# Optimization experiments

Hardware: AMD Instinct MI355X
Metric: run time of the kernel (lower is better)

## Reference

```python
import jax, jax.numpy as jnp
import numpy as np

B, S, H = 8, 1024, 768
NH, DH = 12, 64
F, E = 3072, 8
EPS = 1e-12

def layer_norm(x, g, b):
    mu = jnp.mean(x, axis=-1, keepdims=True)
    var = jnp.var(x, axis=-1, keepdims=True)
    return g * (x - mu) / jnp.sqrt(var + EPS) + b

def setup_inputs():
    key = jax.random.key(0)
    ks = jax.random.split(key, 20)
    std = 0.02
    d = {
        'hidden_states': jax.random.normal(ks[0], (B, S, H), jnp.float32),
        'Wq': jax.random.normal(ks[1], (H, H)) * std, 'bq': jnp.zeros((H,)),
        'Wk': jax.random.normal(ks[2], (H, H)) * std, 'bk': jnp.zeros((H,)),
        'Wv': jax.random.normal(ks[3], (H, H)) * std, 'bv': jnp.zeros((H,)),
        'Wao': jax.random.normal(ks[4], (H, H)) * std, 'bao': jnp.zeros((H,)),
        'ln1_g': jnp.ones((H,)), 'ln1_b': jnp.zeros((H,)),
        'Wr': jax.random.normal(ks[5], (H, E)) * std, 'br': jnp.zeros((E,)),
        'Wi': jax.random.normal(ks[6], (E, H, F)) * std, 'bi': jnp.zeros((E, F)),
        'Wo': jax.random.normal(ks[7], (F, H)) * std, 'bo': jnp.zeros((H,)),
        'ln2_g': jnp.ones((H,)), 'ln2_b': jnp.zeros((H,)),
    }
    return d

def reference(hidden_states, Wq, bq, Wk, bk, Wv, bv, Wao, bao, ln1_g, ln1_b,
              Wr, br, Wi, bi, Wo, bo, ln2_g, ln2_b):
    b, s, h = hidden_states.shape
    # --- self attention ---
    q = (hidden_states @ Wq + bq).reshape(b, s, NH, DH)
    k = (hidden_states @ Wk + bk).reshape(b, s, NH, DH)
    v = (hidden_states @ Wv + bv).reshape(b, s, NH, DH)
    scores = jnp.einsum('bqhd,bkhd->bhqk', q, k) / jnp.sqrt(jnp.float32(DH))
    probs = jax.nn.softmax(scores, axis=-1)
    ctx = jnp.einsum('bhqk,bkhd->bqhd', probs, v).reshape(b, s, h)
    attention_output = layer_norm(ctx @ Wao + bao + hidden_states, ln1_g, ln1_b)
    # --- router ---
    routing_scores = jax.nn.softmax(attention_output @ Wr + br, axis=-1)  # [b,s,E]
    routing_expert = jnp.argmax(routing_scores, axis=-1)  # [b,s]
    # --- expert FFN (dispatch/combine via per-expert masking) ---
    flat_x = attention_output.reshape(-1, h)          # [T,H]
    flat_e = routing_expert.reshape(-1)               # [T]
    flat_inter = jnp.zeros((b * s, F), flat_x.dtype)
    for e in range(E):
        mask = (flat_e == e)[:, None].astype(flat_x.dtype)
        y = jax.nn.gelu(flat_x @ Wi[e] + bi[e], approximate=False)
        flat_inter = flat_inter + mask * y
    inter = flat_inter.reshape(b, s, F)
    # --- output (dense + residual layernorm) ---
    layer_output = layer_norm(inter @ Wo + bo + attention_output, ln2_g, ln2_b)
    return layer_output, routing_scores
```

## Files before the change

### kernel.cpp

```cpp
#include <hip/hip_runtime.h>
#include <math.h>
#include <stdint.h>

#define TOKS 8192
#define HDIM 768
#define FDIM 3072
#define NEXP 8
#define NHEAD 12
#define SEQ 1024
#define BATCH 8
#define PERMSZ 9216

typedef __attribute__((ext_vector_type(8))) short s16x8;
typedef __attribute__((ext_vector_type(4))) short s16x4;
typedef __attribute__((ext_vector_type(4))) float f32x4;

__device__ __forceinline__ short f2bf(float f) {
  uint32_t u = __float_as_uint(f);
  uint32_t r = (u + 0x7fffu + ((u >> 16) & 1u)) >> 16;
  return (short)(r & 0xffffu);
}
__device__ __forceinline__ float bf2f(short h) {
  return __uint_as_float(((uint32_t)(uint16_t)h) << 16);
}
__device__ __forceinline__ void gload16(const void* g, void* l) {
  __builtin_amdgcn_global_load_lds(
      (const __attribute__((address_space(1))) uint32_t*)g,
      (__attribute__((address_space(3))) uint32_t*)l, 16, 0, 0);
}
__device__ __forceinline__ void pipe_wait_barrier() {
  asm volatile("s_waitcnt vmcnt(0)" ::: "memory");
  __builtin_amdgcn_s_barrier();
}

__global__ __launch_bounds__(256) void convert_split(
    const float* __restrict__ X, short* __restrict__ Xh, short* __restrict__ Xl, int n4)
{
  const int i = blockIdx.x * 256 + threadIdx.x;
  if (i >= n4) return;
  const float4 v = ((const float4*)X)[i];
  const float a[4] = {v.x, v.y, v.z, v.w};
  s16x4 h, l;
#pragma unroll
  for (int j = 0; j < 4; ++j) {
    h[j] = f2bf(a[j]);
    l[j] = f2bf(a[j] - bf2f(h[j]));
  }
  ((s16x4*)Xh)[i] = h;
  ((s16x4*)Xl)[i] = l;
}

__global__ __launch_bounds__(256) void transpose_split(
    const float* __restrict__ W, short* __restrict__ WTh, short* __restrict__ WTl,
    int K, int N)
{
  __shared__ float t[32][33];
  const int tid = threadIdx.x;
  const int tx = tid & 31, ty = tid >> 5;
  const int n0 = blockIdx.x * 32, k0 = blockIdx.y * 32;
#pragma unroll
  for (int r = 0; r < 4; ++r)
    t[ty + r * 8][tx] = W[(size_t)(k0 + ty + r * 8) * N + n0 + tx];
  __syncthreads();
#pragma unroll
  for (int r = 0; r < 4; ++r) {
    const float v = t[tx][ty + r * 8];
    const short h = f2bf(v);
    WTh[(size_t)(n0 + ty + r * 8) * K + k0 + tx] = h;
    WTl[(size_t)(n0 + ty + r * 8) * K + k0 + tx] = f2bf(v - bf2f(h));
  }
}

__global__ __launch_bounds__(256) void gemm_split_mfma(
    const short* __restrict__ Ah, const short* __restrict__ Al,
    const short* __restrict__ BhT, const short* __restrict__ BlT,
    const float* __restrict__ bias, float* __restrict__ C,
    int N, int K)
{
  __shared__ __align__(16) short lAh[2][4096];
  __shared__ __align__(16) short lAl[2][4096];
  __shared__ __align__(16) short lBh[2][4096];
  __shared__ __align__(16) short lBl[2][4096];
  const int tid = threadIdx.x;
  const int w = tid >> 6, lane = tid & 63;
  const int wr = w >> 1, wc = w & 1;
  const int row0 = blockIdx.y * 128, col0 = blockIdx.x * 128;
  const int sr = lane & 15, kg = lane >> 4;
  const size_t a0 = (size_t)(row0 + 2 * w * 16 + sr) * K + kg * 8;
  const size_t a1 = a0 + (size_t)16 * K;
  const size_t b0 = (size_t)(col0 + 2 * w * 16 + sr) * K + kg * 8;
  const size_t b1 = b0 + (size_t)16 * K;
  const int d0 = (2 * w) * 512, d1 = (2 * w + 1) * 512;
#define STAGE_S(bu, k0) do { \
    gload16(Ah + a0 + (k0), &lAh[bu][d0]); \
    gload16(Ah + a1 + (k0), &lAh[bu][d1]); \
    gload16(Al + a0 + (k0), &lAl[bu][d0]); \
    gload16(Al + a1 + (k0), &lAl[bu][d1]); \
    gload16(BhT + b0 + (k0), &lBh[bu][d0]); \
    gload16(BhT + b1 + (k0), &lBh[bu][d1]); \
    gload16(BlT + b0 + (k0), &lBl[bu][d0]); \
    gload16(BlT + b1 + (k0), &lBl[bu][d1]); \
  } while (0)
  f32x4 acc[4][4] = {};
  const int NT = K >> 5;
  STAGE_S(0, 0);
  pipe_wait_barrier();
  int cur = 0;
  for (int t = 0; t < NT; ++t) {
    if (t + 1 < NT) STAGE_S(cur ^ 1, (t + 1) * 32);
    s16x8 ah[4], al[4], bh[4], bl[4];
#pragma unroll
    for (int i = 0; i < 4; ++i) {
      ah[i] = *(const s16x8*)&lAh[cur][(wr * 4 + i) * 512 + lane * 8];
      al[i] = *(const s16x8*)&lAl[cur][(wr * 4 + i) * 512 + lane * 8];
      bh[i] = *(const s16x8*)&lBh[cur][(wc * 4 + i) * 512 + lane * 8];
      bl[i] = *(const s16x8*)&lBl[cur][(wc * 4 + i) * 512 + lane * 8];
    }
#pragma unroll
    for (int mi = 0; mi < 4; ++mi)
#pragma unroll
      for (int ni = 0; ni < 4; ++ni) {
        acc[mi][ni] = __builtin_amdgcn_mfma_f32_16x16x32_bf16(ah[mi], bh[ni], acc[mi][ni], 0, 0, 0);
        acc[mi][ni] = __builtin_amdgcn_mfma_f32_16x16x32_bf16(ah[mi], bl[ni], acc[mi][ni], 0, 0, 0);
        acc[mi][ni] = __builtin_amdgcn_mfma_f32_16x16x32_bf16(al[mi], bh[ni], acc[mi][ni], 0, 0, 0);
      }
    pipe_wait_barrier();
    cur ^= 1;
  }
#undef STAGE_S
  const int cl = lane & 15, rg = lane >> 4;
#pragma unroll
  for (int mi = 0; mi < 4; ++mi)
#pragma unroll
    for (int r = 0; r < 4; ++r) {
      const int row = row0 + wr * 64 + mi * 16 + rg * 4 + r;
#pragma unroll
      for (int ni = 0; ni < 4; ++ni) {
        const int c = col0 + wc * 64 + ni * 16 + cl;
        C[(size_t)row * N + c] = acc[mi][ni][r] + bias[c];
      }
    }
}

__global__ __launch_bounds__(256) void qkv_split_mfma(
    const short* __restrict__ Ah, const short* __restrict__ Al,
    const short* __restrict__ BhT, const short* __restrict__ BlT,
    const float* __restrict__ bias,
    short* __restrict__ QKh, short* __restrict__ QKl,
    short* __restrict__ VTh, short* __restrict__ VTl)
{
  const int K = 768;
  __shared__ __align__(16) short lAh[2][4096];
  __shared__ __align__(16) short lAl[2][4096];
  __shared__ __align__(16) short lBh[2][4096];
  __shared__ __align__(16) short lBl[2][4096];
  const int tid = threadIdx.x;
  const int w = tid >> 6, lane = tid & 63;
  const int wr = w >> 1, wc = w & 1;
  const int row0 = blockIdx.y * 128, col0 = blockIdx.x * 128;
  const int sr = lane & 15, kg = lane >> 4;
  const size_t a0 = (size_t)(row0 + 2 * w * 16 + sr) * K + kg * 8;
  const size_t a1 = a0 + (size_t)16 * K;
  const size_t b0 = (size_t)(col0 + 2 * w * 16 + sr) * K + kg * 8;
  const size_t b1 = b0 + (size_t)16 * K;
  const int d0 = (2 * w) * 512, d1 = (2 * w + 1) * 512;
#define STAGE_Q(bu, k0) do { \
    gload16(Ah + a0 + (k0), &lAh[bu][d0]); \
    gload16(Ah + a1 + (k0), &lAh[bu][d1]); \
    gload16(Al + a0 + (k0), &lAl[bu][d0]); \
    gload16(Al + a1 + (k0), &lAl[bu][d1]); \
    gload16(BhT + b0 + (k0), &lBh[bu][d0]); \
    gload16(BhT + b1 + (k0), &lBh[bu][d1]); \
    gload16(BlT + b0 + (k0), &lBl[bu][d0]); \
    gload16(BlT + b1 + (k0), &lBl[bu][d1]); \
  } while (0)
  f32x4 acc[4][4] = {};
  STAGE_Q(0, 0);
  pipe_wait_barrier();
  int cur = 0;
  for (int t = 0; t < 24; ++t) {
    if (t < 23) STAGE_Q(cur ^ 1, (t + 1) * 32);
    s16x8 ah[4], al[4], bh[4], bl[4];
#pragma unroll
    for (int i = 0; i < 4; ++i) {
      ah[i] = *(const s16x8*)&lAh[cur][(wr * 4 + i) * 512 + lane * 8];
      al[i] = *(const s16x8*)&lAl[cur][(wr * 4 + i) * 512 + lane * 8];
      bh[i] = *(const s16x8*)&lBh[cur][(wc * 4 + i) * 512 + lane * 8];
      bl[i] = *(const s16x8*)&lBl[cur][(wc * 4 + i) * 512 + lane * 8];
    }
#pragma unroll
    for (int mi = 0; mi < 4; ++mi)
#pragma unroll
      for (int ni = 0; ni < 4; ++ni) {
        acc[mi][ni] = __builtin_amdgcn_mfma_f32_16x16x32_bf16(ah[mi], bh[ni], acc[mi][ni], 0, 0, 0);
        acc[mi][ni] = __builtin_amdgcn_mfma_f32_16x16x32_bf16(ah[mi], bl[ni], acc[mi][ni], 0, 0, 0);
        acc[mi][ni] = __builtin_amdgcn_mfma_f32_16x16x32_bf16(al[mi], bh[ni], acc[mi][ni], 0, 0, 0);
      }
    pipe_wait_barrier();
    cur ^= 1;
  }
#undef STAGE_Q
  const int cl = lane & 15, rg = lane >> 4;
#pragma unroll
  for (int mi = 0; mi < 4; ++mi)
#pragma unroll
    for (int ni = 0; ni < 4; ++ni) {
      const int c = col0 + wc * 64 + ni * 16 + cl;
      const int rowb = row0 + wr * 64 + mi * 16 + rg * 4;
      s16x4 hv, lv;
#pragma unroll
      for (int r = 0; r < 4; ++r) {
        const float v = acc[mi][ni][r] + bias[c];
        const short hh = f2bf(v);
        hv[r] = hh;
        lv[r] = f2bf(v - bf2f(hh));
      }
      if (c < 1536) {
#pragma unroll
        for (int r = 0; r < 4; ++r) {
          QKh[(size_t)(rowb + r) * 1536 + c] = hv[r];
          QKl[(size_t)(rowb + r) * 1536 + c] = lv[r];
        }
      } else {
        const int dall = c - 1536;
        const size_t vi = (((size_t)((rowb >> 10) * NHEAD + (dall >> 6))) * 64 + (dall & 63)) * 1024
                          + (rowb & 1023);
        *(s16x4*)(VTh + vi) = hv;
        *(s16x4*)(VTl + vi) = lv;
      }
    }
}

__global__ __launch_bounds__(256, 2) void attention_part(
    const short* __restrict__ QKh, const short* __restrict__ QKl,
    const short* __restrict__ VTh, const short* __restrict__ VTl,
    float* __restrict__ O0, float* __restrict__ O1,
    float2* __restrict__ ml0, float2* __restrict__ ml1)
{
  __shared__ __align__(16) short lPh[4][2560];
  __shared__ __align__(16) short lPl[4][2560];
  const int tid = threadIdx.x;
  const int w = tid >> 6, lane = tid & 63;
  const int b = blockIdx.z, h = blockIdx.y;
  const int z = blockIdx.x & 1;
  const int q0 = (blockIdx.x >> 1) * 128 + w * 32;
  const int kv0 = z * 512;
  const int sr = lane & 15, kg = lane >> 4;
  const int cl = sr, rg = kg;
  short* myPh = lPh[w];
  short* myPl = lPl[w];
  float* Op = z ? O1 : O0;
  float2* mlp = z ? ml1 : ml0;

  s16x8 qh[2][2], ql[2][2];
  {
    const size_t qbase = ((size_t)b * SEQ + q0 + sr) * 1536 + h * 64 + kg * 8;
#pragma unroll
    for (int mi = 0; mi < 2; ++mi)
#pragma unroll
      for (int ks = 0; ks < 2; ++ks) {
        const size_t o = qbase + (size_t)mi * (16 * 1536) + ks * 32;
        qh[mi][ks] = *(const s16x8*)(QKh + o);
        ql[mi][ks] = *(const s16x8*)(QKl + o);
      }
  }
  float m_run[2][4], l_run[2][4];
#pragma unroll
  for (int mi = 0; mi < 2; ++mi)
#pragma unroll
    for (int r = 0; r < 4; ++r) { m_run[mi][r] = -3.0e38f; l_run[mi][r] = 0.f; }
  f32x4 acc_o[2][4] = {};

  for (int kt = kv0; kt < kv0 + 512; kt += 64) {
    s16x8 kh[4][2], kl2[4][2];
    {
      const size_t kbase = ((size_t)b * SEQ + kt + sr) * 1536 + 768 + h * 64 + kg * 8;
#pragma unroll
      for (int ni = 0; ni < 4; ++ni)
#pragma unroll
        for (int ks = 0; ks < 2; ++ks) {
          const size_t o = kbase + (size_t)ni * (16 * 1536) + ks * 32;
          kh[ni][ks] = *(const s16x8*)(QKh + o);
          kl2[ni][ks] = *(const s16x8*)(QKl + o);
        }
    }
    f32x4 accs[2][4] = {};
#pragma unroll
    for (int ks = 0; ks < 2; ++ks)
#pragma unroll
      for (int ni = 0; ni < 4; ++ni)
#pragma unroll
        for (int mi = 0; mi < 2; ++mi) {
          accs[mi][ni] = __builtin_amdgcn_mfma_f32_16x16x32_bf16(qh[mi][ks], kh[ni][ks], accs[mi][ni], 0, 0, 0);
          accs[mi][ni] = __builtin_amdgcn_mfma_f32_16x16x32_bf16(qh[mi][ks], kl2[ni][ks], accs[mi][ni], 0, 0, 0);
          accs[mi][ni] = __builtin_amdgcn_mfma_f32_16x16x32_bf16(ql[mi][ks], kh[ni][ks], accs[mi][ni], 0, 0, 0);
        }
    s16x8 vh[4][2], vl2[4][2];
    {
      const size_t vbase = (((size_t)(b * NHEAD + h)) * 64 + sr) * 1024 + kt + kg * 8;
#pragma unroll
      for (int nd = 0; nd < 4; ++nd)
#pragma unroll
        for (int ks2 = 0; ks2 < 2; ++ks2) {
          const size_t o = vbase + (size_t)nd * (16 * 1024) + ks2 * 32;
          vh[nd][ks2] = *(const s16x8*)(VTh + o);
          vl2[nd][ks2] = *(const s16x8*)(VTl + o);
        }
    }
#pragma unroll
    for (int mi = 0; mi < 2; ++mi)
#pragma unroll
      for (int ni = 0; ni < 4; ++ni)
#pragma unroll
        for (int r = 0; r < 4; ++r)
          accs[mi][ni][r] *= 0.125f;
#pragma unroll
    for (int mi = 0; mi < 2; ++mi)
#pragma unroll
      for (int r = 0; r < 4; ++r) {
        float mx = fmaxf(fmaxf(accs[mi][0][r], accs[mi][1][r]),
                         fmaxf(accs[mi][2][r], accs[mi][3][r]));
        mx = fmaxf(mx, __shfl_xor(mx, 1));
        mx = fmaxf(mx, __shfl_xor(mx, 2));
        mx = fmaxf(mx, __shfl_xor(mx, 4));
        mx = fmaxf(mx, __shfl_xor(mx, 8));
        const float mn = fmaxf(m_run[mi][r], mx);
        const float c = __expf(m_run[mi][r] - mn);
        m_run[mi][r] = mn;
        l_run[mi][r] *= c;
#pragma unroll
        for (int nd = 0; nd < 4; ++nd) acc_o[mi][nd][r] *= c;
        float sum = 0.f;
#pragma unroll
        for (int ni = 0; ni < 4; ++ni) {
          const float p = __expf(accs[mi][ni][r] - mn);
          sum += p;
          const short hh = f2bf(p);
          const int idx = (mi * 2 + (ni >> 1)) * 640 + (rg * 4 + r) * 40 + (ni & 1) * 16 + cl;
          myPh[idx] = hh;
          myPl[idx] = f2bf(p - bf2f(hh));
        }
        sum += __shfl_xor(sum, 1);
        sum += __shfl_xor(sum, 2);
        sum += __shfl_xor(sum, 4);
        sum += __shfl_xor(sum, 8);
        l_run[mi][r] += sum;
      }
#pragma unroll
    for (int ks2 = 0; ks2 < 2; ++ks2) {
      s16x8 pf[2], pg[2];
#pragma unroll
      for (int mi = 0; mi < 2; ++mi) {
        const int ra = (mi * 2 + ks2) * 640 + sr * 40 + kg * 8;
        pf[mi] = *(const s16x8*)&myPh[ra];
        pg[mi] = *(const s16x8*)&myPl[ra];
      }
#pragma unroll
      for (int nd = 0; nd < 4; ++nd)
#pragma unroll
        for (int mi = 0; mi < 2; ++mi) {
          acc_o[mi][nd] = __builtin_amdgcn_mfma_f32_16x16x32_bf16(pf[mi], vh[nd][ks2], acc_o[mi][nd], 0, 0, 0);
          acc_o[mi][nd] = __builtin_amdgcn_mfma_f32_16x16x32_bf16(pf[mi], vl2[nd][ks2], acc_o[mi][nd], 0, 0, 0);
          acc_o[mi][nd] = __builtin_amdgcn_mfma_f32_16x16x32_bf16(pg[mi], vh[nd][ks2], acc_o[mi][nd], 0, 0, 0);
        }
    }
  }
#pragma unroll
  for (int mi = 0; mi < 2; ++mi)
#pragma unroll
    for (int nd = 0; nd < 4; ++nd)
#pragma unroll
      for (int r = 0; r < 4; ++r) {
        const int row = q0 + mi * 16 + rg * 4 + r;
        const int d = h * 64 + nd * 16 + cl;
        Op[((size_t)b * SEQ + row) * HDIM + d] = acc_o[mi][nd][r];
      }
  if (sr == 0) {
#pragma unroll
    for (int mi = 0; mi < 2; ++mi)
#pragma unroll
      for (int r = 0; r < 4; ++r) {
        const int row = q0 + mi * 16 + rg * 4 + r;
        mlp[(size_t)(b * NHEAD + h) * SEQ + row] = make_float2(m_run[mi][r], l_run[mi][r]);
      }
  }
}

__global__ __launch_bounds__(256) void attn_combine(
    float* __restrict__ O0, const float* __restrict__ O1,
    const float2* __restrict__ ml0, const float2* __restrict__ ml1)
{
  const int t = blockIdx.x;
  const int b = t >> 10, s = t & 1023;
  const int tid = threadIdx.x;
#pragma unroll
  for (int i = 0; i < 3; ++i) {
    const int idx = tid + i * 256;
    const int h = idx >> 6;
    const float2 a0 = ml0[(size_t)(b * NHEAD + h) * SEQ + s];
    const float2 a1 = ml1[(size_t)(b * NHEAD + h) * SEQ + s];
    const float mm = fmaxf(a0.x, a1.x);
    const float w0 = __expf(a0.x - mm), w1 = __expf(a1.x - mm);
    const float denom = a0.y * w0 + a1.y * w1;
    const size_t o = (size_t)t * HDIM + idx;
    O0[o] = (O0[o] * w0 + O1[o] * w1) / denom;
  }
}

__global__ __launch_bounds__(256) void convert_bf16(
    const float* __restrict__ X, short* __restrict__ Y, int n4)
{
  const int i = blockIdx.x * 256 + threadIdx.x;
  if (i >= n4) return;
  const float4 v = ((const float4*)X)[i];
  s16x4 s;
  s[0] = f2bf(v.x); s[1] = f2bf(v.y); s[2] = f2bf(v.z); s[3] = f2bf(v.w);
  ((s16x4*)Y)[i] = s;
}

__global__ __launch_bounds__(256) void transpose_to_bf16(
    const float* __restrict__ W, short* __restrict__ WT, int K, int N)
{
  const size_t off = (size_t)blockIdx.z * (size_t)K * N;
  const float* Wp = W + off;
  short* WTp = WT + off;
  __shared__ float t[32][33];
  const int tid = threadIdx.x;
  const int tx = tid & 31, ty = tid >> 5;
  const int n0 = blockIdx.x * 32, k0 = blockIdx.y * 32;
#pragma unroll
  for (int r = 0; r < 4; ++r)
    t[ty + r * 8][tx] = Wp[(size_t)(k0 + ty + r * 8) * N + n0 + tx];
  __syncthreads();
#pragma unroll
  for (int r = 0; r < 4; ++r)
    WTp[(size_t)(n0 + ty + r * 8) * K + k0 + tx] = f2bf(t[tx][ty + r * 8]);
}

__global__ __launch_bounds__(256) void expert_up_mfma(
    const short* __restrict__ Abf, const short* __restrict__ WiT,
    const float* __restrict__ bi, const int* __restrict__ perm,
    const int* __restrict__ offs, short* __restrict__ interb)
{
  const int row0 = blockIdx.x * 128;
  if (row0 >= offs[NEXP]) return;
  int e = 0;
  while (offs[e + 1] <= row0) ++e;
  __shared__ __align__(16) short lA[2][4096];
  __shared__ __align__(16) short lB[2][4096];
  __shared__ int toks[128];
  const int tid = threadIdx.x;
  const int w = tid >> 6, lane = tid & 63;
  const int wr = w >> 1, wc = w & 1;
  const int col0 = blockIdx.y * 128;
  if (tid < 128) toks[tid] = perm[row0 + tid];
  __syncthreads();
  const int sr = lane & 15, kg = lane >> 4;
  int t0 = toks[2 * w * 16 + sr];        if (t0 < 0) t0 = toks[0];
  int t1 = toks[(2 * w + 1) * 16 + sr];  if (t1 < 0) t1 = toks[0];
  const size_t a0 = (size_t)t0 * HDIM + kg * 8;
  const size_t a1 = (size_t)t1 * HDIM + kg * 8;
  const short* Bt = WiT + (size_t)e * FDIM * HDIM;
  const size_t b0 = (size_t)(col0 + 2 * w * 16 + sr) * HDIM + kg * 8;
  const size_t b1 = b0 + (size_t)16 * HDIM;
  const int d0 = (2 * w) * 512, d1 = (2 * w + 1) * 512;
#define STAGE_E(bu, k0) do { \
    gload16(Abf + a0 + (k0), &lA[bu][d0]); \
    gload16(Abf + a1 + (k0), &lA[bu][d1]); \
    gload16(Bt + b0 + (k0), &lB[bu][d0]); \
    gload16(Bt + b1 + (k0), &lB[bu][d1]); \
  } while (0)
  f32x4 acc[4][4] = {};
  STAGE_E(0, 0);
  pipe_wait_barrier();
  int cur = 0;
  for (int t = 0; t < 24; ++t) {
    if (t < 23) STAGE_E(cur ^ 1, (t + 1) * 32);
    s16x8 af[4], bg[4];
#pragma unroll
    for (int i = 0; i < 4; ++i) {
      af[i] = *(const s16x8*)&lA[cur][(wr * 4 + i) * 512 + lane * 8];
      bg[i] = *(const s16x8*)&lB[cur][(wc * 4 + i) * 512 + lane * 8];
    }
#pragma unroll
    for (int mi = 0; mi < 4; ++mi)
#pragma unroll
      for (int ni = 0; ni < 4; ++ni)
        acc[mi][ni] = __builtin_amdgcn_mfma_f32_16x16x32_bf16(af[mi], bg[ni], acc[mi][ni], 0, 0, 0);
    pipe_wait_barrier();
    cur ^= 1;
  }
#undef STAGE_E
  const int cl = lane & 15, rg = lane >> 4;
#pragma unroll
  for (int mi = 0; mi < 4; ++mi) {
#pragma unroll
    for (int r = 0; r < 4; ++r) {
      const int rl = wr * 64 + mi * 16 + rg * 4 + r;
      const int tok = toks[rl];
      if (tok < 0) continue;
#pragma unroll
      for (int ni = 0; ni < 4; ++ni) {
        const int c = col0 + wc * 64 + ni * 16 + cl;
        float v = acc[mi][ni][r] + bi[(size_t)e * FDIM + c];
        v = 0.5f * v * (1.0f + erff(v * 0.70710678118654752f));
        interb[(size_t)tok * FDIM + c] = f2bf(v);
      }
    }
  }
}

__global__ __launch_bounds__(256) void wo_mfma(
    const short* __restrict__ Ab, const short* __restrict__ BT,
    const float* __restrict__ bias, float* __restrict__ C0, float* __restrict__ C1)
{
  __shared__ __align__(16) short lA[2][4096];
  __shared__ __align__(16) short lB[2][4096];
  const int tid = threadIdx.x;
  const int w = tid >> 6, lane = tid & 63;
  const int wr = w >> 1, wc = w & 1;
  const int row0 = blockIdx.y * 128, col0 = blockIdx.x * 128;
  const int z = blockIdx.z;
  const int kbase = z * 1536;
  const int sr = lane & 15, kg = lane >> 4;
  const size_t a0 = (size_t)(row0 + 2 * w * 16 + sr) * FDIM + kbase + kg * 8;
  const size_t a1 = a0 + (size_t)16 * FDIM;
  const size_t b0 = (size_t)(col0 + 2 * w * 16 + sr) * FDIM + kbase + kg * 8;
  const size_t b1 = b0 + (size_t)16 * FDIM;
  const int d0 = (2 * w) * 512, d1 = (2 * w + 1) * 512;
#define STAGE_W(bu, k0) do { \
    gload16(Ab + a0 + (k0), &lA[bu][d0]); \
    gload16(Ab + a1 + (k0), &lA[bu][d1]); \
    gload16(BT + b0 + (k0), &lB[bu][d0]); \
    gload16(BT + b1 + (k0), &lB[bu][d1]); \
  } while (0)
  f32x4 acc[4][4] = {};
  STAGE_W(0, 0);
  pipe_wait_barrier();
  int cur = 0;
  for (int t = 0; t < 48; ++t) {
    if (t < 47) STAGE_W(cur ^ 1, (t + 1) * 32);
    s16x8 af[4], bg[4];
#pragma unroll
    for (int i = 0; i < 4; ++i) {
      af[i] = *(const s16x8*)&lA[cur][(wr * 4 + i) * 512 + lane * 8];
      bg[i] = *(const s16x8*)&lB[cur][(wc * 4 + i) * 512 + lane * 8];
    }
#pragma unroll
    for (int mi = 0; mi < 4; ++mi)
#pragma unroll
      for (int ni = 0; ni < 4; ++ni)
        acc[mi][ni] = __builtin_amdgcn_mfma_f32_16x16x32_bf16(af[mi], bg[ni], acc[mi][ni], 0, 0, 0);
    pipe_wait_barrier();
    cur ^= 1;
  }
#undef STAGE_W
  float* C = z ? C1 : C0;
  const int cl = lane & 15, rg = lane >> 4;
#pragma unroll
  for (int mi = 0; mi < 4; ++mi) {
#pragma unroll
    for (int r = 0; r < 4; ++r) {
      const int row = row0 + wr * 64 + mi * 16 + rg * 4 + r;
#pragma unroll
      for (int ni = 0; ni < 4; ++ni) {
        const int c = col0 + wc * 64 + ni * 16 + cl;
        C[(size_t)row * HDIM + c] = acc[mi][ni][r] + (z ? 0.f : bias[c]);
      }
    }
  }
}

__global__ __launch_bounds__(256) void add_ln_kernel(
    const float* __restrict__ X, const float* __restrict__ R,
    const float* __restrict__ g, const float* __restrict__ bb,
    float* __restrict__ out)
{
  const int t = blockIdx.x;
  const int tid = threadIdx.x;
  const float* x = X + (size_t)t * HDIM;
  const float* r = R + (size_t)t * HDIM;
  float v[3];
  float sum = 0.f, ssq = 0.f;
#pragma unroll
  for (int i = 0; i < 3; ++i) {
    const float val = x[tid + i * 256] + r[tid + i * 256];
    v[i] = val;
    sum += val;
    ssq += val * val;
  }
#pragma unroll
  for (int o = 32; o > 0; o >>= 1) {
    sum += __shfl_down(sum, o);
    ssq += __shfl_down(ssq, o);
  }
  __shared__ float red[10];
  const int wid = tid >> 6, lane = tid & 63;
  if (lane == 0) { red[wid] = sum; red[4 + wid] = ssq; }
  __syncthreads();
  if (tid == 0) {
    const float s = red[0] + red[1] + red[2] + red[3];
    const float q = red[4] + red[5] + red[6] + red[7];
    const float mean = s * (1.f / HDIM);
    const float var = q * (1.f / HDIM) - mean * mean;
    red[8] = mean;
    red[9] = rsqrtf(fmaxf(var, 0.f) + 1e-12f);
  }
  __syncthreads();
  const float mean = red[8], rstd = red[9];
#pragma unroll
  for (int i = 0; i < 3; ++i) {
    const int idx = tid + i * 256;
    out[(size_t)t * HDIM + idx] = g[idx] * (v[i] - mean) * rstd + bb[idx];
  }
}

__global__ __launch_bounds__(256) void add2_ln_kernel(
    const float* __restrict__ X1, const float* __restrict__ X2,
    const float* __restrict__ R, const float* __restrict__ g,
    const float* __restrict__ bb, float* __restrict__ out)
{
  const int t = blockIdx.x;
  const int tid = threadIdx.x;
  const float* x1 = X1 + (size_t)t * HDIM;
  const float* x2 = X2 + (size_t)t * HDIM;
  const float* r = R + (size_t)t * HDIM;
  float v[3];
  float sum = 0.f, ssq = 0.f;
#pragma unroll
  for (int i = 0; i < 3; ++i) {
    const float val = x1[tid + i * 256] + x2[tid + i * 256] + r[tid + i * 256];
    v[i] = val;
    sum += val;
    ssq += val * val;
  }
#pragma unroll
  for (int o = 32; o > 0; o >>= 1) {
    sum += __shfl_down(sum, o);
    ssq += __shfl_down(ssq, o);
  }
  __shared__ float red[10];
  const int wid = tid >> 6, lane = tid & 63;
  if (lane == 0) { red[wid] = sum; red[4 + wid] = ssq; }
  __syncthreads();
  if (tid == 0) {
    const float s = red[0] + red[1] + red[2] + red[3];
    const float q = red[4] + red[5] + red[6] + red[7];
    const float mean = s * (1.f / HDIM);
    const float var = q * (1.f / HDIM) - mean * mean;
    red[8] = mean;
    red[9] = rsqrtf(fmaxf(var, 0.f) + 1e-12f);
  }
  __syncthreads();
  const float mean = red[8], rstd = red[9];
#pragma unroll
  for (int i = 0; i < 3; ++i) {
    const int idx = tid + i * 256;
    out[(size_t)t * HDIM + idx] = g[idx] * (v[i] - mean) * rstd + bb[idx];
  }
}

__global__ __launch_bounds__(256) void router_kernel(
    const float* __restrict__ X, const float* __restrict__ Wr,
    const float* __restrict__ br, float* __restrict__ scores_out,
    int* __restrict__ expert, int* __restrict__ counts)
{
  const int wid = threadIdx.x >> 6, lane = threadIdx.x & 63;
  const int tok = blockIdx.x * 4 + wid;
  const float* x = X + (size_t)tok * HDIM;
  float acc[8] = {};
  for (int k0 = 0; k0 < HDIM; k0 += 64) {
    const float xv = x[k0 + lane];
    const float* wrow = Wr + (size_t)(k0 + lane) * NEXP;
    const float4 w0 = *reinterpret_cast<const float4*>(wrow);
    const float4 w1 = *reinterpret_cast<const float4*>(wrow + 4);
    acc[0] = fmaf(xv, w0.x, acc[0]);
    acc[1] = fmaf(xv, w0.y, acc[1]);
    acc[2] = fmaf(xv, w0.z, acc[2]);
    acc[3] = fmaf(xv, w0.w, acc[3]);
    acc[4] = fmaf(xv, w1.x, acc[4]);
    acc[5] = fmaf(xv, w1.y, acc[5]);
    acc[6] = fmaf(xv, w1.z, acc[6]);
    acc[7] = fmaf(xv, w1.w, acc[7]);
  }
#pragma unroll
  for (int e = 0; e < 8; ++e)
#pragma unroll
    for (int o = 32; o > 0; o >>= 1) acc[e] += __shfl_down(acc[e], o);
  if (lane == 0) {
    float mx = -3.0e38f;
#pragma unroll
    for (int e = 0; e < 8; ++e) { acc[e] += br[e]; mx = fmaxf(mx, acc[e]); }
    float sum = 0.f;
#pragma unroll
    for (int e = 0; e < 8; ++e) { acc[e] = expf(acc[e] - mx); sum += acc[e]; }
    const float inv = 1.f / sum;
    int best = 0;
    float bv = acc[0];
#pragma unroll
    for (int e = 0; e < 8; ++e) {
      const float p = acc[e] * inv;
      scores_out[(size_t)tok * NEXP + e] = p;
      if (acc[e] > bv) { bv = acc[e]; best = e; }
    }
    expert[tok] = best;
    atomicAdd(&counts[best], 1);
  }
}

__global__ void offsets_kernel(const int* __restrict__ counts, int* __restrict__ offs)
{
  if (threadIdx.x == 0 && blockIdx.x == 0) {
    int a = 0;
    for (int e = 0; e < NEXP; ++e) {
      offs[e] = a;
      a += ((counts[e] + 127) >> 7) << 7;
    }
    offs[NEXP] = a;
  }
}

__global__ __launch_bounds__(256) void scatter_kernel(
    const int* __restrict__ expert, const int* __restrict__ offs,
    int* __restrict__ cursor, int* __restrict__ perm)
{
  const int t = blockIdx.x * 256 + threadIdx.x;
  if (t >= TOKS) return;
  const int e = expert[t];
  const int pos = atomicAdd(&cursor[e], 1);
  perm[offs[e] + pos] = t;
}

extern "C" void kernel_launch(void* const* d_in, const int* in_sizes, int n_in,
                              void* d_out, int out_size, void* d_ws, size_t ws_size,
                              hipStream_t stream) {
  const float* hidden = (const float*)d_in[0];
  const float* Wq  = (const float*)d_in[1];
  const float* bq  = (const float*)d_in[2];
  const float* Wk  = (const float*)d_in[3];
  const float* bk  = (const float*)d_in[4];
  const float* Wv  = (const float*)d_in[5];
  const float* bv  = (const float*)d_in[6];
  const float* Wao = (const float*)d_in[7];
  const float* bao = (const float*)d_in[8];
  const float* ln1g = (const float*)d_in[9];
  const float* ln1b = (const float*)d_in[10];
  const float* Wr  = (const float*)d_in[11];
  const float* br  = (const float*)d_in[12];
  const float* Wi  = (const float*)d_in[13];
  const float* bi  = (const float*)d_in[14];
  const float* Wo  = (const float*)d_in[15];
  const float* bo  = (const float*)d_in[16];
  const float* ln2g = (const float*)d_in[17];
  const float* ln2b = (const float*)d_in[18];

  float* out = (float*)d_out;
  float* scores_out = out + (size_t)TOKS * HDIM;

  const size_t M1 = (size_t)TOKS * HDIM;
  const size_t HW = (size_t)HDIM * HDIM;
  float* ws = (float*)d_ws;
  short* QKhb = (short*)ws;
  short* QKlb = (short*)(ws + M1);
  short* VThb = (short*)(ws + 2 * M1);
  short* VTlb = VThb + (size_t)BATCH * NHEAD * 64 * 1024;
  float* ctxb = ws + 3 * M1;
  float* Opart1 = ws + 4 * M1;
  float* bqkv = ws + 3 * M1;
  short* Hh = (short*)(ws + 4 * M1);
  short* Hl = Hh + M1;
  short* Ch = Hh; short* Cl = Hl;
  short* wt = (short*)(ws + 5 * M1);
  short* WqkvhT = wt;
  short* WqkvlT = wt + 3 * HW;
  short* WaohT  = wt + 6 * HW;
  short* WaolT  = wt + 7 * HW;
  float2* ml0 = (float2*)(ws + 5 * M1 + 4 * HW);
  float2* ml1 = ml0 + (size_t)BATCH * NHEAD * SEQ;
  float* aoproj   = ws;
  float* attn_out = ws + M1;
  float* tmp2a    = ws;
  float* tmp2b    = ws + 3 * M1;
  short* Abf    = (short*)(ws + 2 * M1);
  short* WiT    = Abf + M1;
  short* WoT    = WiT + (size_t)NEXP * FDIM * HDIM;
  short* interb = WoT + (size_t)HDIM * FDIM;
  int* ints   = (int*)(interb + (size_t)TOKS * FDIM);
  int* perm   = ints;
  int* expert = ints + PERMSZ;
  int* counts = expert + TOKS;
  int* offs   = counts + NEXP;
  int* cursor = offs + NEXP + 1;

  hipMemsetAsync(counts, 0, (NEXP + NEXP + 1 + NEXP) * sizeof(int), stream);
  hipMemsetAsync(perm, 0xFF, PERMSZ * sizeof(int), stream);
  hipMemcpyAsync(bqkv,        bq, HDIM * sizeof(float), hipMemcpyDeviceToDevice, stream);
  hipMemcpyAsync(bqkv + 768,  bk, HDIM * sizeof(float), hipMemcpyDeviceToDevice, stream);
  hipMemcpyAsync(bqkv + 1536, bv, HDIM * sizeof(float), hipMemcpyDeviceToDevice, stream);

  const dim3 blk(256);
  convert_split<<<dim3(TOKS * HDIM / 4 / 256), blk, 0, stream>>>(hidden, Hh, Hl, TOKS * HDIM / 4);
  transpose_split<<<dim3(24, 24), blk, 0, stream>>>(Wq,  WqkvhT,          WqkvlT,          HDIM, HDIM);
  transpose_split<<<dim3(24, 24), blk, 0, stream>>>(Wk,  WqkvhT + HW,     WqkvlT + HW,     HDIM, HDIM);
  transpose_split<<<dim3(24, 24), blk, 0, stream>>>(Wv,  WqkvhT + 2 * HW, WqkvlT + 2 * HW, HDIM, HDIM);
  transpose_split<<<dim3(24, 24), blk, 0, stream>>>(Wao, WaohT,           WaolT,           HDIM, HDIM);

  qkv_split_mfma<<<dim3(2304 / 128, TOKS / 128), blk, 0, stream>>>(
      Hh, Hl, WqkvhT, WqkvlT, bqkv, QKhb, QKlb, VThb, VTlb);

  attention_part<<<dim3((SEQ / 128) * 2, NHEAD, BATCH), blk, 0, stream>>>(
      QKhb, QKlb, VThb, VTlb, ctxb, Opart1, ml0, ml1);
  attn_combine<<<dim3(TOKS), blk, 0, stream>>>(ctxb, Opart1, ml0, ml1);

  convert_split<<<dim3(TOKS * HDIM / 4 / 256), blk, 0, stream>>>(ctxb, Ch, Cl, TOKS * HDIM / 4);
  gemm_split_mfma<<<dim3(HDIM / 128, TOKS / 128), blk, 0, stream>>>(
      Ch, Cl, WaohT, WaolT, bao, aoproj, HDIM, HDIM);
  add_ln_kernel<<<dim3(TOKS), blk, 0, stream>>>(aoproj, hidden, ln1g, ln1b, attn_out);

  router_kernel<<<dim3(TOKS / 4), blk, 0, stream>>>(attn_out, Wr, br, scores_out, expert, counts);
  offsets_kernel<<<dim3(1), dim3(64), 0, stream>>>(counts, offs);
  scatter_kernel<<<dim3(TOKS / 256), blk, 0, stream>>>(expert, offs, cursor, perm);

  transpose_to_bf16<<<dim3(FDIM / 32, HDIM / 32, NEXP), blk, 0, stream>>>(Wi, WiT, HDIM, FDIM);
  transpose_to_bf16<<<dim3(HDIM / 32, FDIM / 32, 1), blk, 0, stream>>>(Wo, WoT, FDIM, HDIM);
  convert_bf16<<<dim3(TOKS * HDIM / 4 / 256), blk, 0, stream>>>(attn_out, Abf, TOKS * HDIM / 4);

  expert_up_mfma<<<dim3(PERMSZ / 128, FDIM / 128), blk, 0, stream>>>(
      Abf, WiT, bi, perm, offs, interb);
  wo_mfma<<<dim3(HDIM / 128, TOKS / 128, 2), blk, 0, stream>>>(interb, WoT, bo, tmp2a, tmp2b);
  add2_ln_kernel<<<dim3(TOKS), blk, 0, stream>>>(tmp2a, tmp2b, attn_out, ln2g, ln2b, out);
}
```

Baseline: 896.9 us.

## Fuse attention combine with bf16 split, split-K output projection, direct A loads

The attention combine kernel now writes the hi/lo bf16 split of the context directly, which removes a separate fp32 store and convert pass. The output projection GEMM becomes a split-K kernel with two K halves written to separate buffers, and the existing add2 layernorm kernel sums them. The QKV and projection GEMMs now read A fragments straight from global memory into registers instead of staging them through LDS, which halves LDS traffic but relies on cache hits for the A reads. Workspace buffers are remapped so the new split outputs do not alias live data.

After: 946.6 us. 5.5% more time.

```diff
diff --git a/kernel.cpp b/kernel.cpp
--- a/kernel.cpp
+++ b/kernel.cpp
@@ -71,14 +71,14 @@
   }
 }
 
-__global__ __launch_bounds__(256) void gemm_split_mfma(
+__global__ __launch_bounds__(256) void qkv_split_mfma(
     const short* __restrict__ Ah, const short* __restrict__ Al,
     const short* __restrict__ BhT, const short* __restrict__ BlT,
-    const float* __restrict__ bias, float* __restrict__ C,
-    int N, int K)
-{
-  __shared__ __align__(16) short lAh[2][4096];
-  __shared__ __align__(16) short lAl[2][4096];
+    const float* __restrict__ bias,
+    short* __restrict__ QKh, short* __restrict__ QKl,
+    short* __restrict__ VTh, short* __restrict__ VTl)
+{
+  const int K = 768;
   __shared__ __align__(16) short lBh[2][4096];
   __shared__ __align__(16) short lBl[2][4096];
   const int tid = threadIdx.x;
@@ -86,33 +86,33 @@
   const int wr = w >> 1, wc = w & 1;
   const int row0 = blockIdx.y * 128, col0 = blockIdx.x * 128;
   const int sr = lane & 15, kg = lane >> 4;
-  const size_t a0 = (size_t)(row0 + 2 * w * 16 + sr) * K + kg * 8;
-  const size_t a1 = a0 + (size_t)16 * K;
+  size_t aoff[4];
+#pragma unroll
+  for (int i = 0; i < 4; ++i)
+    aoff[i] = (size_t)(row0 + (wr * 4 + i) * 16 + sr) * K + kg * 8;
   const size_t b0 = (size_t)(col0 + 2 * w * 16 + sr) * K + kg * 8;
   const size_t b1 = b0 + (size_t)16 * K;
   const int d0 = (2 * w) * 512, d1 = (2 * w + 1) * 512;
-#define STAGE_S(bu, k0) do { \
-    gload16(Ah + a0 + (k0), &lAh[bu][d0]); \
-    gload16(Ah + a1 + (k0), &lAh[bu][d1]); \
-    gload16(Al + a0 + (k0), &lAl[bu][d0]); \
-    gload16(Al + a1 + (k0), &lAl[bu][d1]); \
+#define STAGE_QB(bu, k0) do { \
     gload16(BhT + b0 + (k0), &lBh[bu][d0]); \
     gload16(BhT + b1 + (k0), &lBh[bu][d1]); \
     gload16(BlT + b0 + (k0), &lBl[bu][d0]); \
     gload16(BlT + b1 + (k0), &lBl[bu][d1]); \
   } while (0)
   f32x4 acc[4][4] = {};
-  const int NT = K >> 5;
-  STAGE_S(0, 0);
+  STAGE_QB(0, 0);
   pipe_wait_barrier();
   int cur = 0;
-  for (int t = 0; t < NT; ++t) {
-    if (t + 1 < NT) STAGE_S(cur ^ 1, (t + 1) * 32);
+  for (int t = 0; t < 24; ++t) {
+    if (t < 23) STAGE_QB(cur ^ 1, (t + 1) * 32);
     s16x8 ah[4], al[4], bh[4], bl[4];
 #pragma unroll
     for (int i = 0; i < 4; ++i) {
-      ah[i] = *(const s16x8*)&lAh[cur][(wr * 4 + i) * 512 + lane * 8];
-      al[i] = *(const s16x8*)&lAl[cur][(wr * 4 + i) * 512 + lane * 8];
+      ah[i] = *(const s16x8*)(Ah + aoff[i] + t * 32);
+      al[i] = *(const s16x8*)(Al + aoff[i] + t * 32);
+    }
+#pragma unroll
+    for (int i = 0; i < 4; ++i) {
       bh[i] = *(const s16x8*)&lBh[cur][(wc * 4 + i) * 512 + lane * 8];
       bl[i] = *(const s16x8*)&lBl[cur][(wc * 4 + i) * 512 + lane * 8];
     }
@@ -127,79 +127,7 @@
     pipe_wait_barrier();
     cur ^= 1;
   }
-#undef STAGE_S
-  const int cl = lane & 15, rg = lane >> 4;
-#pragma unroll
-  for (int mi = 0; mi < 4; ++mi)
-#pragma unroll
-    for (int r = 0; r < 4; ++r) {
-      const int row = row0 + wr * 64 + mi * 16 + rg * 4 + r;
-#pragma unroll
-      for (int ni = 0; ni < 4; ++ni) {
-        const int c = col0 + wc * 64 + ni * 16 + cl;
-        C[(size_t)row * N + c] = acc[mi][ni][r] + bias[c];
-      }
-    }
-}
-
-__global__ __launch_bounds__(256) void qkv_split_mfma(
-    const short* __restrict__ Ah, const short* __restrict__ Al,
-    const short* __restrict__ BhT, const short* __restrict__ BlT,
-    const float* __restrict__ bias,
-    short* __restrict__ QKh, short* __restrict__ QKl,
-    short* __restrict__ VTh, short* __restrict__ VTl)
-{
-  const int K = 768;
-  __shared__ __align__(16) short lAh[2][4096];
-  __shared__ __align__(16) short lAl[2][4096];
-  __shared__ __align__(16) short lBh[2][4096];
-  __shared__ __align__(16) short lBl[2][4096];
-  const int tid = threadIdx.x;
-  const int w = tid >> 6, lane = tid & 63;
-  const int wr = w >> 1, wc = w & 1;
-  const int row0 = blockIdx.y * 128, col0 = blockIdx.x * 128;
-  const int sr = lane & 15, kg = lane >> 4;
-  const size_t a0 = (size_t)(row0 + 2 * w * 16 + sr) * K + kg * 8;
-  const size_t a1 = a0 + (size_t)16 * K;
-  const size_t b0 = (size_t)(col0 + 2 * w * 16 + sr) * K + kg * 8;
-  const size_t b1 = b0 + (size_t)16 * K;
-  const int d0 = (2 * w) * 512, d1 = (2 * w + 1) * 512;
-#define STAGE_Q(bu, k0) do { \
-    gload16(Ah + a0 + (k0), &lAh[bu][d0]); \
-    gload16(Ah + a1 + (k0), &lAh[bu][d1]); \
-    gload16(Al + a0 + (k0), &lAl[bu][d0]); \
-    gload16(Al + a1 + (k0), &lAl[bu][d1]); \
-    gload16(BhT + b0 + (k0), &lBh[bu][d0]); \
-    gload16(BhT + b1 + (k0), &lBh[bu][d1]); \
-    gload16(BlT + b0 + (k0), &lBl[bu][d0]); \
-    gload16(BlT + b1 + (k0), &lBl[bu][d1]); \
-  } while (0)
-  f32x4 acc[4][4] = {};
-  STAGE_Q(0, 0);
-  pipe_wait_barrier();
-  int cur = 0;
-  for (int t = 0; t < 24; ++t) {
-    if (t < 23) STAGE_Q(cur ^ 1, (t + 1) * 32);
-    s16x8 ah[4], al[4], bh[4], bl[4];
-#pragma unroll
-    for (int i = 0; i < 4; ++i) {
-      ah[i] = *(const s16x8*)&lAh[cur][(wr * 4 + i) * 512 + lane * 8];
-      al[i] = *(const s16x8*)&lAl[cur][(wr * 4 + i) * 512 + lane * 8];
-      bh[i] = *(const s16x8*)&lBh[cur][(wc * 4 + i) * 512 + lane * 8];
-      bl[i] = *(const s16x8*)&lBl[cur][(wc * 4 + i) * 512 + lane * 8];
-    }
-#pragma unroll
-    for (int mi = 0; mi < 4; ++mi)
-#pragma unroll
-      for (int ni = 0; ni < 4; ++ni) {
-        acc[mi][ni] = __builtin_amdgcn_mfma_f32_16x16x32_bf16(ah[mi], bh[ni], acc[mi][ni], 0, 0, 0);
-        acc[mi][ni] = __builtin_amdgcn_mfma_f32_16x16x32_bf16(ah[mi], bl[ni], acc[mi][ni], 0, 0, 0);
-        acc[mi][ni] = __builtin_amdgcn_mfma_f32_16x16x32_bf16(al[mi], bh[ni], acc[mi][ni], 0, 0, 0);
-      }
-    pipe_wait_barrier();
-    cur ^= 1;
-  }
-#undef STAGE_Q
+#undef STAGE_QB
   const int cl = lane & 15, rg = lane >> 4;
 #pragma unroll
   for (int mi = 0; mi < 4; ++mi)
@@ -227,6 +155,79 @@
                           + (rowb & 1023);
         *(s16x4*)(VTh + vi) = hv;
         *(s16x4*)(VTl + vi) = lv;
+      }
+    }
+}
+
+__global__ __launch_bounds__(256) void gemm_splitk_mfma(
+    const short* __restrict__ Ah, const short* __restrict__ Al,
+    const short* __restrict__ BhT, const short* __restrict__ BlT,
+    const float* __restrict__ bias, float* __restrict__ C0, float* __restrict__ C1,
+    int N, int K)
+{
+  __shared__ __align__(16) short lBh[2][4096];
+  __shared__ __align__(16) short lBl[2][4096];
+  const int tid = threadIdx.x;
+  const int w = tid >> 6, lane = tid & 63;
+  const int wr = w >> 1, wc = w & 1;
+  const int row0 = blockIdx.y * 128, col0 = blockIdx.x * 128;
+  const int z = blockIdx.z;
+  const int Khalf = K >> 1, koff = z * Khalf;
+  const int sr = lane & 15, kg = lane >> 4;
+  size_t aoff[4];
+#pragma unroll
+  for (int i = 0; i < 4; ++i)
+    aoff[i] = (size_t)(row0 + (wr * 4 + i) * 16 + sr) * K + koff + kg * 8;
+  const size_t b0 = (size_t)(col0 + 2 * w * 16 + sr) * K + koff + kg * 8;
+  const size_t b1 = b0 + (size_t)16 * K;
+  const int d0 = (2 * w) * 512, d1 = (2 * w + 1) * 512;
+#define STAGE_KB(bu, k0) do { \
+    gload16(BhT + b0 + (k0), &lBh[bu][d0]); \
+    gload16(BhT + b1 + (k0), &lBh[bu][d1]); \
+    gload16(BlT + b0 + (k0), &lBl[bu][d0]); \
+    gload16(BlT + b1 + (k0), &lBl[bu][d1]); \
+  } while (0)
+  f32x4 acc[4][4] = {};
+  const int NT = Khalf >> 5;
+  STAGE_KB(0, 0);
+  pipe_wait_barrier();
+  int cur = 0;
+  for (int t = 0; t < NT; ++t) {
+    if (t + 1 < NT) STAGE_KB(cur ^ 1, (t + 1) * 32);
+    s16x8 ah[4], al[4], bh[4], bl[4];
+#pragma unroll
+    for (int i = 0; i < 4; ++i) {
+      ah[i] = *(const s16x8*)(Ah + aoff[i] + t * 32);
+      al[i] = *(const s16x8*)(Al + aoff[i] + t * 32);
+    }
+#pragma unroll
+    for (int i = 0; i < 4; ++i) {
+      bh[i] = *(const s16x8*)&lBh[cur][(wc * 4 + i) * 512 + lane * 8];
+      bl[i] = *(const s16x8*)&lBl[cur][(wc * 4 + i) * 512 + lane * 8];
+    }
+#pragma unroll
+    for (int mi = 0; mi < 4; ++mi)
+#pragma unroll
+      for (int ni = 0; ni < 4; ++ni) {
+        acc[mi][ni] = __builtin_amdgcn_mfma_f32_16x16x32_bf16(ah[mi], bh[ni], acc[mi][ni], 0, 0, 0);
+        acc[mi][ni] = __builtin_amdgcn_mfma_f32_16x16x32_bf16(ah[mi], bl[ni], acc[mi][ni], 0, 0, 0);
+        acc[mi][ni] = __builtin_amdgcn_mfma_f32_16x16x32_bf16(al[mi], bh[ni], acc[mi][ni], 0, 0, 0);
+      }
+    pipe_wait_barrier();
+    cur ^= 1;
+  }
+#undef STAGE_KB
+  float* C = z ? C1 : C0;
+  const int cl = lane & 15, rg = lane >> 4;
+#pragma unroll
+  for (int mi = 0; mi < 4; ++mi)
+#pragma unroll
+    for (int r = 0; r < 4; ++r) {
+      const int row = row0 + wr * 64 + mi * 16 + rg * 4 + r;
+#pragma unroll
+      for (int ni = 0; ni < 4; ++ni) {
+        const int c = col0 + wc * 64 + ni * 16 + cl;
+        C[(size_t)row * N + c] = acc[mi][ni][r] + (z ? 0.f : bias[c]);
       }
     }
 }
@@ -386,9 +387,10 @@
   }
 }
 
-__global__ __launch_bounds__(256) void attn_combine(
-    float* __restrict__ O0, const float* __restrict__ O1,
-    const float2* __restrict__ ml0, const float2* __restrict__ ml1)
+__global__ __launch_bounds__(256) void combine_split(
+    const float* __restrict__ O0, const float* __restrict__ O1,
+    const float2* __restrict__ ml0, const float2* __restrict__ ml1,
+    short* __restrict__ Ch, short* __restrict__ Cl)
 {
   const int t = blockIdx.x;
   const int b = t >> 10, s = t & 1023;
@@ -403,7 +405,10 @@
     const float w0 = __expf(a0.x - mm), w1 = __expf(a1.x - mm);
     const float denom = a0.y * w0 + a1.y * w1;
     const size_t o = (size_t)t * HDIM + idx;
-    O0[o] = (O0[o] * w0 + O1[o] * w1) / denom;
+    const float v = (O0[o] * w0 + O1[o] * w1) / denom;
+    const short hh = f2bf(v);
+    Ch[o] = hh;
+    Cl[o] = f2bf(v - bf2f(hh));
   }
 }
 
@@ -571,50 +576,6 @@
   }
 }
 
-__global__ __launch_bounds__(256) void add_ln_kernel(
-    const float* __restrict__ X, const float* __restrict__ R,
-    const float* __restrict__ g, const float* __restrict__ bb,
-    float* __restrict__ out)
-{
-  const int t = blockIdx.x;
-  const int tid = threadIdx.x;
-  const float* x = X + (size_t)t * HDIM;
-  const float* r = R + (size_t)t * HDIM;
-  float v[3];
-  float sum = 0.f, ssq = 0.f;
-#pragma unroll
-  for (int i = 0; i < 3; ++i) {
-    const float val = x[tid + i * 256] + r[tid + i * 256];
-    v[i] = val;
-    sum += val;
-    ssq += val * val;
-  }
-#pragma unroll
-  for (int o = 32; o > 0; o >>= 1) {
-    sum += __shfl_down(sum, o);
-    ssq += __shfl_down(ssq, o);
-  }
-  __shared__ float red[10];
-  const int wid = tid >> 6, lane = tid & 63;
-  if (lane == 0) { red[wid] = sum; red[4 + wid] = ssq; }
-  __syncthreads();
-  if (tid == 0) {
-    const float s = red[0] + red[1] + red[2] + red[3];
-    const float q = red[4] + red[5] + red[6] + red[7];
-    const float mean = s * (1.f / HDIM);
-    const float var = q * (1.f / HDIM) - mean * mean;
-    red[8] = mean;
-    red[9] = rsqrtf(fmaxf(var, 0.f) + 1e-12f);
-  }
-  __syncthreads();
-  const float mean = red[8], rstd = red[9];
-#pragma unroll
-  for (int i = 0; i < 3; ++i) {
-    const int idx = tid + i * 256;
-    out[(size_t)t * HDIM + idx] = g[idx] * (v[i] - mean) * rstd + bb[idx];
-  }
-}
-
 __global__ __launch_bounds__(256) void add2_ln_kernel(
     const float* __restrict__ X1, const float* __restrict__ X2,
     const float* __restrict__ R, const float* __restrict__ g,
@@ -764,12 +725,13 @@
   short* QKlb = (short*)(ws + M1);
   short* VThb = (short*)(ws + 2 * M1);
   short* VTlb = VThb + (size_t)BATCH * NHEAD * 64 * 1024;
-  float* ctxb = ws + 3 * M1;
-  float* Opart1 = ws + 4 * M1;
+  float* O0b  = ws + 3 * M1;
+  float* O1b  = ws + 4 * M1;
   float* bqkv = ws + 3 * M1;
   short* Hh = (short*)(ws + 4 * M1);
   short* Hl = Hh + M1;
-  short* Ch = Hh; short* Cl = Hl;
+  short* Ch = (short*)(ws + 2 * M1);
+  short* Cl = Ch + M1;
   short* wt = (short*)(ws + 5 * M1);
   short* WqkvhT = wt;
   short* WqkvlT = wt + 3 * HW;
@@ -777,7 +739,8 @@
   short* WaolT  = wt + 7 * HW;
   float2* ml0 = (float2*)(ws + 5 * M1 + 4 * HW);
   float2* ml1 = ml0 + (size_t)BATCH * NHEAD * SEQ;
-  float* aoproj   = ws;
+  float* aoproj0  = ws;
+  float* aoproj1  = ws + 3 * M1;
   float* attn_out = ws + M1;
   float* tmp2a    = ws;
   float* tmp2b    = ws + 3 * M1;
@@ -809,13 +772,12 @@
       Hh, Hl, WqkvhT, WqkvlT, bqkv, QKhb, QKlb, VThb, VTlb);
 
   attention_part<<<dim3((SEQ / 128) * 2, NHEAD, BATCH), blk, 0, stream>>>(
-      QKhb, QKlb, VThb, VTlb, ctxb, Opart1, ml0, ml1);
-  attn_combine<<<dim3(TOKS), blk, 0, stream>>>(ctxb, Opart1, ml0, ml1);
-
-  convert_split<<<dim3(TOKS * HDIM / 4 / 256), blk, 0, stream>>>(ctxb, Ch, Cl, TOKS * HDIM / 4);
-  gemm_split_mfma<<<dim3(HDIM / 128, TOKS / 128), blk, 0, stream>>>(
-      Ch, Cl, WaohT, WaolT, bao, aoproj, HDIM, HDIM);
-  add_ln_kernel<<<dim3(TOKS), blk, 0, stream>>>(aoproj, hidden, ln1g, ln1b, attn_out);
+      QKhb, QKlb, VThb, VTlb, O0b, O1b, ml0, ml1);
+  combine_split<<<dim3(TOKS), blk, 0, stream>>>(O0b, O1b, ml0, ml1, Ch, Cl);
+
+  gemm_splitk_mfma<<<dim3(HDIM / 128, TOKS / 128, 2), blk, 0, stream>>>(
+      Ch, Cl, WaohT, WaolT, bao, aoproj0, aoproj1, HDIM, HDIM);
+  add2_ln_kernel<<<dim3(TOKS), blk, 0, stream>>>(aoproj0, aoproj1, hidden, ln1g, ln1b, attn_out);
 
   router_kernel<<<dim3(TOKS / 4), blk, 0, stream>>>(attn_out, Wr, br, scores_out, expert, counts);
   offsets_kernel<<<dim3(1), dim3(64), 0, stream>>>(counts, offs);
```
